# Kernel tuning notes

Hardware: AMD Instinct MI355X
Metric: run time of the kernel (lower is better)

The kernel has to match this reference:

```python
import jax, jax.numpy as jnp
import numpy as np


def setup_inputs() -> dict:
    key = jax.random.key(0)
    k1, k2, k3 = jax.random.split(key, 3)
    B, D, F, P = 4096, 1024, 2048, 1024
    return {
        "x": jax.random.normal(k1, (B, D), dtype=jnp.float32),
        "features": jax.random.normal(k2, (F, D), dtype=jnp.float32),
        "prototypes": jax.random.normal(k3, (P, D), dtype=jnp.float32),
        "alpha": jnp.ones((1,), dtype=jnp.float32),
        "beta": jnp.ones((1,), dtype=jnp.float32),
        "theta": jnp.ones((1,), dtype=jnp.float32),
    }


def reference(x, features, prototypes, alpha, beta, theta):
    # Project each set ONCE (the original redundantly broadcasts first).
    xf = x @ features.T            # [B, F]
    pf = prototypes @ features.T   # [P, F]
    sx = jax.nn.sigmoid(xf)        # x_present [B, F]
    sp = jax.nn.sigmoid(pf)        # p_present [P, F]
    ax = xf * sx                   # [B, F]
    bp = pf * sp                   # [P, F]
    # common[b,p]        = sum_f xf*pf*sx*sp            = (xf*sx) @ (pf*sp)^T
    # x_distinct[b,p]    = sum_f xf*sx*(1-sp)           = rowsum(xf*sx) - (xf*sx) @ sp^T
    # p_distinct[b,p]    = sum_f pf*sp*(1-sx)           = rowsum(pf*sp) - sx @ (pf*sp)^T
    common = ax @ bp.T                                     # [B, P]
    x_distinctive = ax.sum(axis=1, keepdims=True) - ax @ sp.T  # [B, P]
    p_distinctive = bp.sum(axis=1)[None, :] - sx @ bp.T        # [B, P]
    return theta * common - alpha * x_distinctive - beta * p_distinctive
```

## Files before the change

### kernel.cpp

```cpp
#include <hip/hip_runtime.h>
#include <hip/hip_bf16.h>

typedef __bf16 bf16_t;
typedef bf16_t bf16x4 __attribute__((ext_vector_type(4)));
typedef bf16_t bf16x8 __attribute__((ext_vector_type(8)));
typedef float f32x4 __attribute__((ext_vector_type(4)));

#define AS1 __attribute__((address_space(1)))
#define AS3 __attribute__((address_space(3)))

__device__ __forceinline__ void gload_lds16(const void* g, void* l) {
    __builtin_amdgcn_global_load_lds((const AS1 void*)g, (AS3 void*)l, 16, 0, 0);
}
__device__ __forceinline__ void gload_lds4(const void* g, void* l) {
    __builtin_amdgcn_global_load_lds((const AS1 void*)g, (AS3 void*)l, 4, 0, 0);
}

__device__ __forceinline__ float sigmoidf_(float v) {
    return 1.0f / (1.0f + __expf(-v));
}

__global__ __launch_bounds__(256) void k_convert3(const float* __restrict__ x,
                                                  const float* __restrict__ pr,
                                                  const float* __restrict__ ft,
                                                  bf16_t* __restrict__ XPs,
                                                  bf16_t* __restrict__ F16s) {
    const int n4 = 7168 * 256;
    int i = blockIdx.x * 256 + threadIdx.x;
    const int stride = gridDim.x * 256;
    for (; i < n4; i += stride) {
        float4 v;
        long r;
        int c4;
        bf16_t* dst;
        long R;
        if (i < 1048576) {
            v = ((const float4*)x)[i];
            r = i >> 8; c4 = i & 255; dst = XPs; R = 5120;
        } else if (i < 1310720) {
            const int j = i - 1048576;
            v = ((const float4*)pr)[j];
            r = 4096 + (j >> 8); c4 = j & 255; dst = XPs; R = 5120;
        } else {
            const int j = i - 1310720;
            v = ((const float4*)ft)[j];
            r = j >> 8; c4 = j & 255; dst = F16s; R = 2048;
        }
        const int col = c4 << 2;
        const int kb = col >> 5;
        const int cw = col & 31;
        bf16x4 o;
        o[0] = (bf16_t)v.x; o[1] = (bf16_t)v.y; o[2] = (bf16_t)v.z; o[3] = (bf16_t)v.w;
        *(bf16x4*)(dst + ((long)kb * R + r) * 32 + cw) = o;
    }
}

__global__ __launch_bounds__(256) void k_reduce4(const bf16_t* __restrict__ part,
                                                 const float* __restrict__ rsPart,
                                                 const float* __restrict__ pa,
                                                 float* __restrict__ out) {
    const int blk = blockIdx.x;
    const int t = threadIdx.x;
    const int idx = blk * 256 + t;
    const int region = idx >> 13;
    const int widx = idx & 8191;
    const int wv = widx >> 10;
    const int chunk = (widx >> 6) & 15;
    const int ln = widx & 63;
    const int bx = region >> 2, by = region & 3;
    const int wm = wv >> 1 >> 1, wn = wv & 3;
    const int fg = chunk >> 1, gp = chunk & 1;
    const int er = (ln >> 4) << 2, ec = ln & 15;
    const long off = (long)idx * 8;
    const int c = blk & 31;

    __shared__ float rowsum[32];
    __shared__ float colsum[64];
    const int base_r = bx * 256 + wm * 128 + (c & 3) * 32;
    const int base_c = by * 256 + wn * 64;
    if (t < 32) {
        float s = 0.f;
#pragma unroll
        for (int b = 0; b < 8; ++b) s += rsPart[b * 5120 + base_r + t];
        rowsum[t] = pa[0] * s;
    } else if (t < 96) {
        const int cc = t - 32;
        float s = 0.f;
#pragma unroll
        for (int b = 0; b < 8; ++b) s += rsPart[b * 5120 + 4096 + base_c + cc];
        colsum[cc] = s;
    }

    float sum[8] = {};
#pragma unroll
    for (int s = 0; s < 4; ++s) {
        bf16x8 v = *(const bf16x8*)(part + (long)s * 4194304 + off);
#pragma unroll
        for (int j = 0; j < 8; ++j) sum[j] += (float)v[j];
    }
    __syncthreads();

    const int r0 = bx * 256 + wm * 128 + fg * 16 + er;
    const int c0 = by * 256 + wn * 64 + gp * 32 + ec;
#pragma unroll
    for (int q = 0; q < 4; ++q) {
        const float ra = rowsum[r0 + q - base_r];
#pragma unroll
        for (int gh = 0; gh < 2; ++gh) {
            const int col = c0 + gh * 16;
            out[(long)(r0 + q) * 1024 + col] = sum[gh * 4 + q] - ra - colsum[col - base_c];
        }
    }
}

__global__ __launch_bounds__(512, 2) void gemm2_8p(
    const bf16_t* __restrict__ A2s, const bf16_t* __restrict__ B2s,
    bf16_t* __restrict__ O1, long zstride) {
    __shared__ char lds[131072];
    const int tid = threadIdx.x;
    const int wave = tid >> 6, lane = tid & 63;
    const int wm = wave >> 2, wn = wave & 3;

    const int gx = gridDim.x, gy = gridDim.y;
    const int o = blockIdx.x + gx * (blockIdx.y + gy * blockIdx.z);
    const int cpx = (gx * gy * (int)gridDim.z) >> 3;
    const int v = (o & 7) * cpx + (o >> 3);
    const int bx = v % gx;
    const int rem = v / gx;
    const int by = rem % gy;
    const int bz = rem / gy;

    const long bm = (long)bx * 256, bn = (long)by * 256;
    const int kb32_0 = bz * 32;
    const char* Ab = (const char*)A2s;
    const char* Bb = (const char*)B2s;

    const int swzcb = ((lane >> 4) << 4) ^ (((lane >> 3) & 1) << 5);
    const int base_a = (wm * 128 + (lane & 15)) * 64 + swzcb;
    const int base_b = (wn * 64 + (lane & 15)) * 64 + swzcb;

    f32x4 acc[8][4] = {};

    auto STAGEC = [&](const char* gbase, int ldsoff) {
#pragma unroll
        for (int j = 0; j < 2; ++j) {
            const int oo = (j * 512 + tid) << 4;
            const int cb = (oo & 63) ^ (((oo >> 9) & 1) << 5);
            gload_lds16(gbase + (oo & ~63) + cb, lds + ldsoff + (oo & ~1023));
        }
    };

#define VM8 asm volatile("s_waitcnt vmcnt(8)" ::: "memory")
#define VM4 asm volatile("s_waitcnt vmcnt(4)" ::: "memory")
#define VM0 asm volatile("s_waitcnt vmcnt(0)" ::: "memory")

    auto PFETCH = [&](int pf) {
        const long kb = kb32_0 + pf;
        const int ps = pf & 3;
        STAGEC(Ab + (kb * 4096 + bm) * 64, ps * 16384);
        STAGEC(Bb + (kb * 1024 + bn) * 64, 65536 + ps * 16384);
    };

#define PHASE2(p, WAITSTMT, DOPF)                                               \
    do {                                                                        \
        WAITSTMT;                                                               \
        __builtin_amdgcn_s_barrier();                                           \
        __builtin_amdgcn_s_setprio(1);                                          \
        const int slot = (p) & 3;                                               \
        const char* sA = lds + slot * 16384;                                    \
        const char* sB = lds + 65536 + slot * 16384;                            \
        bf16x8 af[8];                                                           \
        bf16x8 bfr[4];                                                          \
        _Pragma("unroll") for (int f = 0; f < 8; ++f)                           \
            af[f] = *(const bf16x8*)(sA + base_a + f * 1024);                   \
        _Pragma("unroll") for (int g = 0; g < 4; ++g)                           \
            bfr[g] = *(const bf16x8*)(sB + base_b + g * 1024);                  \
        if (DOPF) PFETCH((p) + 3);                                              \
        _Pragma("unroll") for (int f = 0; f < 8; ++f)                           \
            _Pragma("unroll") for (int g = 0; g < 4; ++g)                       \
                acc[f][g] = __builtin_amdgcn_mfma_f32_16x16x32_bf16(            \
                    af[f], bfr[g], acc[f][g], 0, 0, 0);                         \
        __builtin_amdgcn_s_setprio(0);                                          \
    } while (0)

    const int NP = 32;
    PFETCH(0);
    PFETCH(1);
    PFETCH(2);

    for (int p = 0; p < NP - 3; ++p) PHASE2(p, VM8, 1);
    PHASE2(NP - 3, VM8, 0);
    PHASE2(NP - 2, VM4, 0);
    PHASE2(NP - 1, VM0, 0);

#undef PHASE2
#undef VM8
#undef VM4
#undef VM0

    bf16_t* Op = O1 + (long)bz * zstride + (long)(bx * 4 + by) * 65536 +
                 wave * 8192 + lane * 8;
#pragma unroll
    for (int fg = 0; fg < 8; ++fg)
#pragma unroll
        for (int gp = 0; gp < 2; ++gp) {
            bf16x8 w;
#pragma unroll
            for (int gh = 0; gh < 2; ++gh)
#pragma unroll
                for (int q = 0; q < 4; ++q)
                    w[gh * 4 + q] = (bf16_t)acc[fg][gp * 2 + gh][q];
            *(bf16x8*)(Op + (fg * 2 + gp) * 512) = w;
        }
}

__global__ __launch_bounds__(512, 2) void gemm1_160(
    const bf16_t* __restrict__ XPs, const bf16_t* __restrict__ F16s,
    bf16_t* __restrict__ A2s, bf16_t* __restrict__ B2s,
    float* __restrict__ rsPart,
    const float* __restrict__ pa, const float* __restrict__ pb,
    const float* __restrict__ pt) {
    __shared__ char lds[106496];
    const int tid = threadIdx.x;
    const int wave = tid >> 6, lane = tid & 63;
    const int wm = wave >> 2, wn = wave & 3;

    const int gx = gridDim.x, gy = gridDim.y;
    const int o = blockIdx.x + gx * blockIdx.y;
    const int cpx = (gx * gy) >> 3;
    const int v = (o & 7) * cpx + (o >> 3);
    const int bx = v % gx;
    const int by = v / gx;

    const long bm = (long)bx * 160, bn = (long)by * 256;
    const char* Ab = (const char*)XPs;
    const char* Bb = (const char*)F16s;

    const int swzcb = ((lane >> 4) << 4) ^ (((lane >> 3) & 1) << 5);
    const int base_a = (wm * 80 + (lane & 15)) * 64 + swzcb;
    const int base_b = (wn * 64 + (lane & 15)) * 64 + swzcb;

    f32x4 acc[5][4] = {};

#define VM8 asm volatile("s_waitcnt vmcnt(8)" ::: "memory")
#define VM4 asm volatile("s_waitcnt vmcnt(4)" ::: "memory")
#define VM0 asm volatile("s_waitcnt vmcnt(0)" ::: "memory")

    auto PFETCH = [&](int pf) {
        const int ps = pf & 3;
        const char* Ag = Ab + ((long)pf * 5120 + bm) * 64;
        const char* Bg = Bb + ((long)pf * 2048 + bn) * 64;
        {
            const int oo = tid << 4;
            const int cb = (oo & 63) ^ (((oo >> 9) & 1) << 5);
            gload_lds16(Ag + (oo & ~63) + cb, lds + ps * 10240 + (oo & ~1023));
        }
        {
            const int oo = 8192 + (tid << 2);
            const int cb = (oo & 63) ^ (((oo >> 9) & 1) << 5);
            gload_lds4(Ag + (oo & ~63) + cb, lds + ps * 10240 + 8192 + wave * 256);
        }
#pragma unroll
        for (int j = 0; j < 2; ++j) {
            const int oo = (j * 512 + tid) << 4;
            const int cb = (oo & 63) ^ (((oo >> 9) & 1) << 5);
            gload_lds16(Bg + (oo & ~63) + cb, lds + 40960 + ps * 16384 + (oo & ~1023));
        }
    };

#define PHASE1(p, WAITSTMT, DOPF)                                               \
    do {                                                                        \
        WAITSTMT;                                                               \
        __builtin_amdgcn_s_barrier();                                           \
        __builtin_amdgcn_s_setprio(1);                                          \
        const int slot = (p) & 3;                                               \
        const char* sA = lds + slot * 10240;                                    \
        const char* sB = lds + 40960 + slot * 16384;                            \
        bf16x8 af[5];                                                           \
        bf16x8 bfr[4];                                                          \
        _Pragma("unroll") for (int f = 0; f < 5; ++f)                           \
            af[f] = *(const bf16x8*)(sA + base_a + f * 1024);                   \
        _Pragma("unroll") for (int g = 0; g < 4; ++g)                           \
            bfr[g] = *(const bf16x8*)(sB + base_b + g * 1024);                  \
        if (DOPF) PFETCH((p) + 3);                                              \
        _Pragma("unroll") for (int f = 0; f < 5; ++f)                           \
            _Pragma("unroll") for (int g = 0; g < 4; ++g)                       \
                acc[f][g] = __builtin_amdgcn_mfma_f32_16x16x32_bf16(            \
                    bfr[g], af[f], acc[f][g], 0, 0, 0);                         \
        __builtin_amdgcn_s_setprio(0);                                          \
    } while (0)

    const int NP = 32;
    PFETCH(0);
    PFETCH(1);
    PFETCH(2);

    for (int p = 0; p < NP - 3; ++p) PHASE1(p, VM8, 1);
    PHASE1(NP - 3, VM8, 0);
    PHASE1(NP - 2, VM4, 0);
    PHASE1(NP - 1, VM0, 0);

#undef PHASE1
#undef VM8
#undef VM4
#undef VM0

    const float va = pa[0], vb = pb[0], vt = pt[0];
    const int lm = lane & 15;
    const int ln4 = (lane >> 4) << 2;
    const int kbbase = (int)(bn >> 5) + wn * 2;
    float rs[5];
#pragma unroll
    for (int f = 0; f < 5; ++f) rs[f] = 0.f;

#pragma unroll
    for (int mf = 0; mf < 5; ++mf) {
        const long grow = bm + wm * 80 + mf * 16 + lm;
        const bool isXf = (grow < 4096);
        const long rowidx = isXf ? grow : (grow - 4096);
        const long rowsz = isXf ? 4096 : 1024;
        bf16_t* base = isXf ? A2s : B2s;
#pragma unroll
        for (int g = 0; g < 4; ++g) {
            bf16x4 w0, w1;
            float rsl = 0.f;
#pragma unroll
            for (int q = 0; q < 4; ++q) {
                const float vv = acc[mf][g][q];
                const float s = sigmoidf_(vv);
                const float prod = vv * s;
                w0[q] = (bf16_t)(isXf ? prod : (vt * prod + va * s));
                w1[q] = (bf16_t)(isXf ? s : (vb * prod));
                rsl += isXf ? prod : vb * prod;
            }
            rs[mf] += rsl;
            const long kb = kbbase + (g >> 1);
            const int c0 = (g & 1) * 16 + ln4;
            *(bf16x4*)(base + (kb * rowsz + rowidx) * 32 + c0) = w0;
            *(bf16x4*)(base + ((kb + 64) * rowsz + rowidx) * 32 + c0) = w1;
        }
    }

    __syncthreads();
    float* lds_f = (float*)lds;
#pragma unroll
    for (int f = 0; f < 5; ++f) {
        float t = rs[f];
        t += __shfl_xor(t, 16);
        t += __shfl_xor(t, 32);
        if ((lane >> 4) == 0) lds_f[wn * 160 + wm * 80 + f * 16 + lm] = t;
    }
    __syncthreads();
    if (tid < 160) {
        const float s = lds_f[tid] + lds_f[160 + tid] + lds_f[320 + tid] + lds_f[480 + tid];
        rsPart[(long)by * 5120 + bm + tid] = s;
    }
}

extern "C" void kernel_launch(void* const* d_in, const int* in_sizes, int n_in,
                              void* d_out, int out_size, void* d_ws, size_t ws_size,
                              hipStream_t stream) {
    const float* x = (const float*)d_in[0];
    const float* feats = (const float*)d_in[1];
    const float* protos = (const float*)d_in[2];
    const float* pa = (const float*)d_in[3];
    const float* pb = (const float*)d_in[4];
    const float* pt = (const float*)d_in[5];
    float* out = (float*)d_out;

    constexpr long Bsz = 4096, D = 1024, F = 2048, P = 1024;

    bf16_t* XPs = (bf16_t*)d_ws;
    bf16_t* F16s = XPs + (Bsz + P) * D;
    bf16_t* A2s = F16s + F * D;
    bf16_t* B2s = A2s + Bsz * 2 * F;
    float* rsPart = (float*)(B2s + P * 2 * F);
    bf16_t* part = (bf16_t*)(rsPart + 8 * 5120);

    k_convert3<<<2048, 256, 0, stream>>>(x, protos, feats, XPs, F16s);

    gemm1_160<<<dim3(32, 8), 512, 0, stream>>>(XPs, F16s, A2s, B2s, rsPart, pa, pb, pt);

    gemm2_8p<<<dim3(Bsz / 256, P / 256, 4), 512, 0, stream>>>(
        A2s, B2s, part, (long)Bsz * P);

    k_reduce4<<<2048, 256, 0, stream>>>(part, rsPart, pa, out);
}
```

Before: 84.16 us.

## Quantize second-stage GEMM operands to FP8 and use FP8 MFMA

The intermediate sigmoid-weighted activations produced by the first GEMM are now packed to FP8 instead of bf16, in a new k-group-major layout. The second GEMM loads these with one 16-byte global-to-LDS copy per operand per stage and runs the fp8 16x16x32 MFMA. This halves the intermediate memory traffic and LDS footprint and uses the higher-throughput FP8 matrix path. The cost is much lower precision on values that feed a large reduction, which may exceed the accuracy tolerance. The unswizzled LDS reads may also cause bank conflicts.

```diff
diff --git a/kernel.cpp b/kernel.cpp
--- a/kernel.cpp
+++ b/kernel.cpp
@@ -68,7 +68,7 @@
     const int chunk = (widx >> 6) & 15;
     const int ln = widx & 63;
     const int bx = region >> 2, by = region & 3;
-    const int wm = wv >> 1 >> 1, wn = wv & 3;
+    const int wm = wv >> 2, wn = wv & 3;
     const int fg = chunk >> 1, gp = chunk & 1;
     const int er = (ln >> 4) << 2, ec = ln & 15;
     const long off = (long)idx * 8;
@@ -114,12 +114,13 @@
 }
 
 __global__ __launch_bounds__(512, 2) void gemm2_8p(
-    const bf16_t* __restrict__ A2s, const bf16_t* __restrict__ B2s,
+    const char* __restrict__ A8, const char* __restrict__ B8,
     bf16_t* __restrict__ O1, long zstride) {
-    __shared__ char lds[131072];
+    __shared__ char lds[65536];
     const int tid = threadIdx.x;
     const int wave = tid >> 6, lane = tid & 63;
     const int wm = wave >> 2, wn = wave & 3;
+    const int lm = lane & 15;
 
     const int gx = gridDim.x, gy = gridDim.y;
     const int o = blockIdx.x + gx * (blockIdx.y + gy * blockIdx.z);
@@ -132,33 +133,25 @@
 
     const long bm = (long)bx * 256, bn = (long)by * 256;
     const int kb32_0 = bz * 32;
-    const char* Ab = (const char*)A2s;
-    const char* Bb = (const char*)B2s;
-
-    const int swzcb = ((lane >> 4) << 4) ^ (((lane >> 3) & 1) << 5);
-    const int base_a = (wm * 128 + (lane & 15)) * 64 + swzcb;
-    const int base_b = (wn * 64 + (lane & 15)) * 64 + swzcb;
+
+    const int base_a = (lane >> 4) * 2048 + (wm * 128 + lm) * 8;
+    const int base_b = (lane >> 4) * 2048 + (wn * 64 + lm) * 8;
 
     f32x4 acc[8][4] = {};
 
-    auto STAGEC = [&](const char* gbase, int ldsoff) {
-#pragma unroll
-        for (int j = 0; j < 2; ++j) {
-            const int oo = (j * 512 + tid) << 4;
-            const int cb = (oo & 63) ^ (((oo >> 9) & 1) << 5);
-            gload_lds16(gbase + (oo & ~63) + cb, lds + ldsoff + (oo & ~1023));
-        }
-    };
-
-#define VM8 asm volatile("s_waitcnt vmcnt(8)" ::: "memory")
 #define VM4 asm volatile("s_waitcnt vmcnt(4)" ::: "memory")
+#define VM2 asm volatile("s_waitcnt vmcnt(2)" ::: "memory")
 #define VM0 asm volatile("s_waitcnt vmcnt(0)" ::: "memory")
 
     auto PFETCH = [&](int pf) {
         const long kb = kb32_0 + pf;
         const int ps = pf & 3;
-        STAGEC(Ab + (kb * 4096 + bm) * 64, ps * 16384);
-        STAGEC(Bb + (kb * 1024 + bn) * 64, 65536 + ps * 16384);
+        const int kg = tid >> 7;
+        const int li = (tid & 127) << 4;
+        gload_lds16(A8 + kb * 131072 + (long)kg * 32768 + bm * 8 + li,
+                    lds + ps * 8192 + wave * 1024);
+        gload_lds16(B8 + kb * 32768 + (long)kg * 8192 + bn * 8 + li,
+                    lds + 32768 + ps * 8192 + wave * 1024);
     };
 
 #define PHASE2(p, WAITSTMT, DOPF)                                               \
@@ -167,18 +160,18 @@
         __builtin_amdgcn_s_barrier();                                           \
         __builtin_amdgcn_s_setprio(1);                                          \
         const int slot = (p) & 3;                                               \
-        const char* sA = lds + slot * 16384;                                    \
-        const char* sB = lds + 65536 + slot * 16384;                            \
-        bf16x8 af[8];                                                           \
-        bf16x8 bfr[4];                                                          \
+        const char* sA = lds + slot * 8192;                                     \
+        const char* sB = lds + 32768 + slot * 8192;                             \
+        long long af[8];                                                        \
+        long long bfr[4];                                                       \
         _Pragma("unroll") for (int f = 0; f < 8; ++f)                           \
-            af[f] = *(const bf16x8*)(sA + base_a + f * 1024);                   \
+            af[f] = *(const long long*)(sA + base_a + f * 128);                 \
         _Pragma("unroll") for (int g = 0; g < 4; ++g)                           \
-            bfr[g] = *(const bf16x8*)(sB + base_b + g * 1024);                  \
+            bfr[g] = *(const long long*)(sB + base_b + g * 128);                \
         if (DOPF) PFETCH((p) + 3);                                              \
         _Pragma("unroll") for (int f = 0; f < 8; ++f)                           \
             _Pragma("unroll") for (int g = 0; g < 4; ++g)                       \
-                acc[f][g] = __builtin_amdgcn_mfma_f32_16x16x32_bf16(            \
+                acc[f][g] = __builtin_amdgcn_mfma_f32_16x16x32_fp8_fp8(         \
                     af[f], bfr[g], acc[f][g], 0, 0, 0);                         \
         __builtin_amdgcn_s_setprio(0);                                          \
     } while (0)
@@ -188,14 +181,14 @@
     PFETCH(1);
     PFETCH(2);
 
-    for (int p = 0; p < NP - 3; ++p) PHASE2(p, VM8, 1);
-    PHASE2(NP - 3, VM8, 0);
-    PHASE2(NP - 2, VM4, 0);
+    for (int p = 0; p < NP - 3; ++p) PHASE2(p, VM4, 1);
+    PHASE2(NP - 3, VM4, 0);
+    PHASE2(NP - 2, VM2, 0);
     PHASE2(NP - 1, VM0, 0);
 
 #undef PHASE2
-#undef VM8
 #undef VM4
+#undef VM2
 #undef VM0
 
     bf16_t* Op = O1 + (long)bz * zstride + (long)(bx * 4 + by) * 65536 +
@@ -216,7 +209,7 @@
 
 __global__ __launch_bounds__(512, 2) void gemm1_160(
     const bf16_t* __restrict__ XPs, const bf16_t* __restrict__ F16s,
-    bf16_t* __restrict__ A2s, bf16_t* __restrict__ B2s,
+    char* __restrict__ A8, char* __restrict__ B8,
     float* __restrict__ rsPart,
     const float* __restrict__ pa, const float* __restrict__ pb,
     const float* __restrict__ pt) {
@@ -319,25 +312,31 @@
         const bool isXf = (grow < 4096);
         const long rowidx = isXf ? grow : (grow - 4096);
         const long rowsz = isXf ? 4096 : 1024;
-        bf16_t* base = isXf ? A2s : B2s;
+        char* base = isXf ? A8 : B8;
 #pragma unroll
         for (int g = 0; g < 4; ++g) {
-            bf16x4 w0, w1;
+            float o0[4], o1[4];
             float rsl = 0.f;
 #pragma unroll
             for (int q = 0; q < 4; ++q) {
                 const float vv = acc[mf][g][q];
                 const float s = sigmoidf_(vv);
                 const float prod = vv * s;
-                w0[q] = (bf16_t)(isXf ? prod : (vt * prod + va * s));
-                w1[q] = (bf16_t)(isXf ? s : (vb * prod));
+                o0[q] = isXf ? prod : (vt * prod + va * s);
+                o1[q] = isXf ? s : (vb * prod);
                 rsl += isXf ? prod : vb * prod;
             }
             rs[mf] += rsl;
+            int u0 = __builtin_amdgcn_cvt_pk_fp8_f32(o0[0], o0[1], 0, false);
+            u0 = __builtin_amdgcn_cvt_pk_fp8_f32(o0[2], o0[3], u0, true);
+            int u1 = __builtin_amdgcn_cvt_pk_fp8_f32(o1[0], o1[1], 0, false);
+            u1 = __builtin_amdgcn_cvt_pk_fp8_f32(o1[2], o1[3], u1, true);
             const long kb = kbbase + (g >> 1);
-            const int c0 = (g & 1) * 16 + ln4;
-            *(bf16x4*)(base + (kb * rowsz + rowidx) * 32 + c0) = w0;
-            *(bf16x4*)(base + ((kb + 64) * rowsz + rowidx) * 32 + c0) = w1;
+            const int fbase = (g & 1) * 16 + ln4;
+            const int kgrp = fbase >> 3;
+            const int sub = fbase & 7;
+            *(int*)(base + ((kb * 4 + kgrp) * rowsz + rowidx) * 8 + sub) = u0;
+            *(int*)(base + (((kb + 64) * 4 + kgrp) * rowsz + rowidx) * 8 + sub) = u1;
         }
     }
 
@@ -372,17 +371,17 @@
 
     bf16_t* XPs = (bf16_t*)d_ws;
     bf16_t* F16s = XPs + (Bsz + P) * D;
-    bf16_t* A2s = F16s + F * D;
-    bf16_t* B2s = A2s + Bsz * 2 * F;
-    float* rsPart = (float*)(B2s + P * 2 * F);
+    char* A8 = (char*)(F16s + F * D);
+    char* B8 = A8 + 128L * 4 * 4096 * 8;
+    float* rsPart = (float*)(B8 + 128L * 4 * 1024 * 8);
     bf16_t* part = (bf16_t*)(rsPart + 8 * 5120);
 
     k_convert3<<<2048, 256, 0, stream>>>(x, protos, feats, XPs, F16s);
 
-    gemm1_160<<<dim3(32, 8), 512, 0, stream>>>(XPs, F16s, A2s, B2s, rsPart, pa, pb, pt);
+    gemm1_160<<<dim3(32, 8), 512, 0, stream>>>(XPs, F16s, A8, B8, rsPart, pa, pb, pt);
 
     gemm2_8p<<<dim3(Bsz / 256, P / 256, 4), 512, 0, stream>>>(
-        A2s, B2s, part, (long)Bsz * P);
+        A8, B8, part, (long)Bsz * P);
 
     k_reduce4<<<2048, 256, 0, stream>>>(part, rsPart, pa, out);
 }
```

New measurement: 79.19 us (median of 2 runs). 5.9% less time.
